# Kernel optimization log

Measured on AMD Instinct MI355X. Metric: run time of the kernel, lower is better.

## Reference

```python
import jax, jax.numpy as jnp
import numpy as np

N = 100_000   # nodes
C = 32        # classes
E = 3_200_000 # edges


def setup_inputs() -> dict:
    key = jax.random.key(0)
    k1, k2, k3, k4, k5 = jax.random.split(key, 5)
    edge_index = jax.random.randint(k1, (2, E), 0, N, dtype=jnp.int32)
    edge_weight = jax.random.uniform(k2, (E,), dtype=jnp.float32) + 0.1  # positive weights
    inputs = jax.random.normal(k3, (N, C), dtype=jnp.float32)
    labels = jax.random.randint(k4, (N,), 0, C)
    y = jax.nn.one_hot(labels, C, dtype=jnp.float32)  # torch.where(y[:, i]) implies one-hot labels
    sample_mask = jax.random.bernoulli(k5, 0.5, (N,))
    return {"edge_index": edge_index, "edge_weight": edge_weight,
            "inputs": inputs, "y": y, "sample_mask": sample_mask}


def _normalize_sparse(edge_index, edge_weight, n):
    # normalize_sparse_tensor: add self-loops (weight 1), then D^{-1/2} A D^{-1/2}
    loop = jnp.arange(n, dtype=edge_index.dtype)
    row = jnp.concatenate([edge_index[0], loop])
    col = jnp.concatenate([edge_index[1], loop])
    w = jnp.concatenate([edge_weight, jnp.ones((n,), edge_weight.dtype)])
    deg = jax.ops.segment_sum(w, row, num_segments=n)
    dinv = jnp.where(deg > 0, jax.lax.rsqrt(deg), 0.0)
    vals = dinv[row] * w * dinv[col]
    return row, col, vals


def reference(edge_index, edge_weight, inputs, y, sample_mask):
    n, c = inputs.shape
    row, col, vals = _normalize_sparse(edge_index, edge_weight, n)

    p = jax.nn.softmax(inputs, axis=1)
    m = sample_mask.astype(p.dtype)[:, None]
    p = p * (1.0 - m) + y * m          # replace predictions by labels on masked nodes
    ym = y * m                          # labels only on masked nodes

    # nodeH = raw_normed_adj @ p   (sparse spmm)  -> (n, c)
    nodeH = jax.ops.segment_sum(vals[:, None] * p[col], row, num_segments=n)

    # per-class mean of nodeH over nodes with label i (one-hot => sum/count)
    cnt = ym.sum(axis=0)                         # (c,)
    H = (ym.T @ nodeH) / cnt[:, None]            # (c, c); NaN rows if class empty

    # NaN fixups (identity when no NaNs present)
    Hn = jnp.isnan(H)
    H = jnp.where(Hn, H.T, H)
    Hn = jnp.isnan(H)
    H0 = jnp.where(Hn, jnp.zeros_like(H), H)
    miss = (1.0 - H0.sum(axis=1, keepdims=True)) / Hn.sum(axis=1, keepdims=True).astype(H.dtype)
    H = jnp.where(Hn, miss, H0)

    # makeDoubleStochasticH: iterate col-norm then row-norm; 'delta' = ||H||_1 (as in source)
    def cond(state):
        _, i, d = state
        return (d >= 1e-12) & (i < 3000)

    def body(state):
        Hc, i, _ = state
        Hc = Hc / Hc.sum(axis=0, keepdims=True)
        Hc = Hc / Hc.sum(axis=1, keepdims=True)
        return Hc, i + 1, jnp.abs(Hc).sum()

    H, _, _ = jax.lax.while_loop(cond, body, (H, jnp.int32(0), jnp.float32(1e30)))
    return H
```

## Files before the change

### kernel.cpp

```cpp
#include <hip/hip_runtime.h>
#include <hip/hip_fp16.h>


#define RS 32768
#define RSH 15
#define BDEG 64
#define NCOPY 16
#define NSC 1024
#define NGE 256

__global__ __launch_bounds__(1024) void
k_deg(const int* __restrict__ ei, const float* __restrict__ ew,
      float* __restrict__ slab, const unsigned char* __restrict__ mask_bytes,
      int* __restrict__ flag, float* __restrict__ T, float* __restrict__ Hg,
      float* __restrict__ cnt, int Nn, int E_, int R) {
  __shared__ float h[RS];
  {
    float4* T4 = (float4*)T;
    int nT4 = Nn * 8;
    float4 z = make_float4(0.f, 0.f, 0.f, 0.f);
    for (int i = blockIdx.x * 1024 + threadIdx.x; i < nT4; i += gridDim.x * 1024)
      T4[i] = z;
  }
  if (blockIdx.x == 0) {
    for (int i = threadIdx.x; i < NCOPY * 1024; i += 1024) Hg[i] = 0.f;
    if (threadIdx.x < 32) cnt[threadIdx.x] = 0.f;
    __shared__ int shi;
    if (threadIdx.x == 0) shi = 0;
    __syncthreads();
    int acc = 0;
    for (int i = threadIdx.x; i < 1024; i += blockDim.x)
      acc |= mask_bytes[i * 4 + 1] | mask_bytes[i * 4 + 2] | mask_bytes[i * 4 + 3];
    if (acc) atomicOr(&shi, 1);
    __syncthreads();
    if (threadIdx.x == 0) *flag = (shi != 0) ? 1 : 0;
  }
  int r = blockIdx.x % R;
  int sl = blockIdx.x / R;
  for (int i = threadIdx.x; i < RS; i += 1024) h[i] = 0.f;
  __syncthreads();
  int lo = r << RSH;
  int Q = E_ >> 2;
  int q0 = (int)((long long)Q * sl / BDEG);
  int q1 = (int)((long long)Q * (sl + 1) / BDEG);
  const int4* ei4 = (const int4*)ei;
  const float4* ew4 = (const float4*)ew;
  int q = q0 + threadIdx.x;
  for (; q + 1024 < q1; q += 2048) {
    int4 ia = ei4[q], ib = ei4[q + 1024];
    float4 wa = ew4[q], wb = ew4[q + 1024];
    unsigned o0 = (unsigned)(ia.x - lo), o1 = (unsigned)(ia.y - lo);
    unsigned o2 = (unsigned)(ia.z - lo), o3 = (unsigned)(ia.w - lo);
    unsigned o4 = (unsigned)(ib.x - lo), o5 = (unsigned)(ib.y - lo);
    unsigned o6 = (unsigned)(ib.z - lo), o7 = (unsigned)(ib.w - lo);
    if (o0 < RS) atomicAdd(&h[o0], wa.x);
    if (o1 < RS) atomicAdd(&h[o1], wa.y);
    if (o2 < RS) atomicAdd(&h[o2], wa.z);
    if (o3 < RS) atomicAdd(&h[o3], wa.w);
    if (o4 < RS) atomicAdd(&h[o4], wb.x);
    if (o5 < RS) atomicAdd(&h[o5], wb.y);
    if (o6 < RS) atomicAdd(&h[o6], wb.z);
    if (o7 < RS) atomicAdd(&h[o7], wb.w);
  }
  for (; q < q1; q += 1024) {
    int4 idx = ei4[q];
    float4 w = ew4[q];
    unsigned o0 = (unsigned)(idx.x - lo), o1 = (unsigned)(idx.y - lo);
    unsigned o2 = (unsigned)(idx.z - lo), o3 = (unsigned)(idx.w - lo);
    if (o0 < RS) atomicAdd(&h[o0], w.x);
    if (o1 < RS) atomicAdd(&h[o1], w.y);
    if (o2 < RS) atomicAdd(&h[o2], w.z);
    if (o3 < RS) atomicAdd(&h[o3], w.w);
  }
  if (sl == BDEG - 1) {
    for (int e = (Q << 2) + threadIdx.x; e < E_; e += 1024) {
      unsigned off = (unsigned)(ei[e] - lo);
      if (off < RS) atomicAdd(&h[off], ew[e]);
    }
  }
  __syncthreads();
  float* dst = slab + ((size_t)r * BDEG + sl) * RS;
  for (int i = threadIdx.x; i < RS; i += 1024) dst[i] = h[i];
}

__global__ void k_node(const float* __restrict__ x, const float* __restrict__ y,
                       const void* __restrict__ maskp, const int* __restrict__ flag,
                       const float* __restrict__ slab, int2* __restrict__ ninfo,
                       __half* __restrict__ p16, float* __restrict__ Hg,
                       float* __restrict__ cnt, int Nn) {
  __shared__ float scnt[32], sdiag[32];
  if (threadIdx.x < 32) { scnt[threadIdx.x] = 0.f; sdiag[threadIdx.x] = 0.f; }
  __syncthreads();
  int n = blockIdx.x * blockDim.x + threadIdx.x;
  if (n < Nn) {
    const float* sl = slab + ((size_t)(n >> RSH) * BDEG) * RS + (n & (RS - 1));
    float d = 0.f;
    #pragma unroll 8
    for (int bb = 0; bb < BDEG; ++bb) d += sl[(size_t)bb * RS];
    float dinv = rsqrtf(d + 1.0f);
    bool byteMask = (*flag != 0);
    bool msk = byteMask ? (((const unsigned char*)maskp)[n] != 0)
                        : (((const int*)maskp)[n] != 0);
    int a = -1;
    if (msk) {
      const float4* yi = (const float4*)(y + (size_t)n * 32);
      #pragma unroll
      for (int q = 0; q < 8; ++q) {
        float4 v = yi[q];
        if (v.x == 1.f) a = q * 4 + 0;
        if (v.y == 1.f) a = q * 4 + 1;
        if (v.z == 1.f) a = q * 4 + 2;
        if (v.w == 1.f) a = q * 4 + 3;
      }
      atomicAdd(&scnt[a], 1.f);
      atomicAdd(&sdiag[a], dinv * dinv);
    } else {
      const float4* xi = (const float4*)(x + (size_t)n * 32);
      float xs[32];
      #pragma unroll
      for (int q = 0; q < 8; ++q) {
        float4 v = xi[q];
        xs[q*4+0] = v.x; xs[q*4+1] = v.y; xs[q*4+2] = v.z; xs[q*4+3] = v.w;
      }
      float mx = -3.4e38f;
      #pragma unroll
      for (int i = 0; i < 32; ++i) mx = fmaxf(mx, xs[i]);
      float s = 0.f;
      #pragma unroll
      for (int i = 0; i < 32; ++i) { xs[i] = __expf(xs[i] - mx); s += xs[i]; }
      float inv = 1.f / s;
      union { short s[32]; int4 v[4]; } u;
      #pragma unroll
      for (int i = 0; i < 32; ++i)
        u.s[i] = __half_as_short(__float2half(xs[i] * inv));
      int4* po = (int4*)(p16 + (size_t)n * 32);
      #pragma unroll
      for (int q = 0; q < 4; ++q) po[q] = u.v[q];
    }
    int2 ni; ni.x = __float_as_int(dinv); ni.y = a;
    ninfo[n] = ni;
  }
  __syncthreads();
  if (threadIdx.x < 32) {
    if (scnt[threadIdx.x] != 0.f) atomicAdd(&cnt[threadIdx.x], scnt[threadIdx.x]);
    if (sdiag[threadIdx.x] != 0.f) atomicAdd(&Hg[threadIdx.x * 33], sdiag[threadIdx.x]);
  }
}

__global__ __launch_bounds__(1024) void
k_scatter(const int* __restrict__ ei, const float* __restrict__ ew,
          const int2* __restrict__ ninfo, float* __restrict__ T,
          float* __restrict__ scatSlab, int E_) {
  __shared__ float sH[1024];
  sH[threadIdx.x] = 0.f;
  __syncthreads();
  int t = blockIdx.x * 1024 + threadIdx.x;
  int stride = gridDim.x * 1024;
  int E4 = E_ >> 2;
  for (int q = t; q < E4; q += stride) {
    int4 rr = ((const int4*)ei)[q];
    int4 cc = ((const int4*)(ei + E_))[q];
    float4 ww = ((const float4*)ew)[q];
    int rs[4] = {rr.x, rr.y, rr.z, rr.w};
    int cs[4] = {cc.x, cc.y, cc.z, cc.w};
    float wv[4] = {ww.x, ww.y, ww.z, ww.w};
    int2 nr[4], nc[4];
    #pragma unroll
    for (int k = 0; k < 4; ++k) nr[k] = ninfo[rs[k]];
    #pragma unroll
    for (int k = 0; k < 4; ++k) nc[k] = ninfo[cs[k]];
    #pragma unroll
    for (int k = 0; k < 4; ++k) {
      if (nr[k].y >= 0) {
        float val = __int_as_float(nr[k].x) * wv[k] * __int_as_float(nc[k].x);
        if (nc[k].y >= 0)
          atomicAdd(&sH[nr[k].y * 32 + nc[k].y], val);
        else
          atomicAdd(&T[(size_t)cs[k] * 32 + nr[k].y], val);
      }
    }
  }
  for (int e = (E4 << 2) + t; e < E_; e += stride) {
    int2 nr = ninfo[ei[e]];
    if (nr.y >= 0) {
      int c = ei[E_ + e];
      int2 nc = ninfo[c];
      float val = __int_as_float(nr.x) * ew[e] * __int_as_float(nc.x);
      if (nc.y >= 0) atomicAdd(&sH[nr.y * 32 + nc.y], val);
      else atomicAdd(&T[(size_t)c * 32 + nr.y], val);
    }
  }
  __syncthreads();
  scatSlab[(size_t)blockIdx.x * 1024 + threadIdx.x] = sH[threadIdx.x];
}

__global__ __launch_bounds__(256) void
k_gemm(const float* __restrict__ T, const __half* __restrict__ p16,
       const float* __restrict__ scatSlab, float* __restrict__ gemmSlab, int Nn) {
  __shared__ float sH[1024];
  for (int i = threadIdx.x; i < 1024; i += 256) sH[i] = 0.f;
  __syncthreads();
  int b = threadIdx.x & 31;
  int hwG = blockIdx.x * 8 + (threadIdx.x >> 5);
  int nHW = gridDim.x * 8;
  int per = (Nn + nHW - 1) / nHW;
  int c0 = hwG * per;
  int c1 = min(c0 + per, Nn);
  float acc[32];
  #pragma unroll
  for (int a = 0; a < 32; ++a) acc[a] = 0.f;
  int c = c0;
  for (; c + 3 < c1; c += 4) {
    float t0 = T[(size_t)(c+0) * 32 + b];
    float t1 = T[(size_t)(c+1) * 32 + b];
    float t2 = T[(size_t)(c+2) * 32 + b];
    float t3 = T[(size_t)(c+3) * 32 + b];
    float p0 = __half2float(p16[(size_t)(c+0) * 32 + b]);
    float p1 = __half2float(p16[(size_t)(c+1) * 32 + b]);
    float p2 = __half2float(p16[(size_t)(c+2) * 32 + b]);
    float p3 = __half2float(p16[(size_t)(c+3) * 32 + b]);
    #pragma unroll
    for (int a = 0; a < 32; ++a)
      acc[a] += __shfl(t0, a, 32) * p0 + __shfl(t1, a, 32) * p1
              + __shfl(t2, a, 32) * p2 + __shfl(t3, a, 32) * p3;
  }
  for (; c < c1; ++c) {
    float tv = T[(size_t)c * 32 + b];
    float pv = __half2float(p16[(size_t)c * 32 + b]);
    #pragma unroll
    for (int a = 0; a < 32; ++a) acc[a] += __shfl(tv, a, 32) * pv;
  }
  #pragma unroll
  for (int a = 0; a < 32; ++a) atomicAdd(&sH[a * 32 + b], acc[a]);
  __syncthreads();
  for (int i = threadIdx.x; i < 1024; i += 256) {
    float v = sH[i];
    #pragma unroll
    for (int k = 0; k < NSC / NGE; ++k)
      v += scatSlab[(size_t)(blockIdx.x + k * NGE) * 1024 + i];
    gemmSlab[(size_t)blockIdx.x * 1024 + i] = v;
  }
}

__global__ __launch_bounds__(1024) void
k_sinkhorn(const float* __restrict__ Hg, const float* __restrict__ gemmSlab,
           const float* __restrict__ cnt, float* __restrict__ out) {
  __shared__ float sHH[1024];
  int t = threadIdx.x;
  float s = 0.f;
  #pragma unroll 8
  for (int k = 0; k < NCOPY; ++k) s += Hg[k * 1024 + t];
  #pragma unroll 8
  for (int k = 0; k < NGE; ++k) s += gemmSlab[k * 1024 + t];
  sHH[t] = s;
  __syncthreads();
  int j = t;
  if (j >= 32) return;
  float cj = cnt[j];
  float Hcol[32], Hrow[32];
  #pragma unroll
  for (int i = 0; i < 32; ++i) Hcol[i] = sHH[i * 32 + j];
  #pragma unroll
  for (int i = 0; i < 32; ++i) Hcol[i] /= __shfl(cj, i);
  #pragma unroll
  for (int k = 0; k < 32; ++k) Hrow[k] = sHH[j * 32 + k] / cj;
  float u = 1.f, v = 1.f;
  for (int it = 0; it < 40; ++it) {
    float a0 = 0.f, a1 = 0.f, a2 = 0.f, a3 = 0.f;
    #pragma unroll
    for (int i = 0; i < 32; i += 4) {
      a0 += Hcol[i+0] * __shfl(u, i+0);
      a1 += Hcol[i+1] * __shfl(u, i+1);
      a2 += Hcol[i+2] * __shfl(u, i+2);
      a3 += Hcol[i+3] * __shfl(u, i+3);
    }
    v = 1.f / ((a0 + a1) + (a2 + a3));
    a0 = a1 = a2 = a3 = 0.f;
    #pragma unroll
    for (int k = 0; k < 32; k += 4) {
      a0 += Hrow[k+0] * __shfl(v, k+0);
      a1 += Hrow[k+1] * __shfl(v, k+1);
      a2 += Hrow[k+2] * __shfl(v, k+2);
      a3 += Hrow[k+3] * __shfl(v, k+3);
    }
    u = 1.f / ((a0 + a1) + (a2 + a3));
  }
  #pragma unroll
  for (int i = 0; i < 32; ++i) out[i * 32 + j] = __shfl(u, i) * Hcol[i] * v;
}

extern "C" void kernel_launch(void* const* d_in, const int* in_sizes, int n_in,
                              void* d_out, int out_size, void* d_ws, size_t ws_size,
                              hipStream_t stream) {
  const int*   ei   = (const int*)d_in[0];
  const float* ew   = (const float*)d_in[1];
  const float* x    = (const float*)d_in[2];
  const float* y    = (const float*)d_in[3];
  const void*  mask = d_in[4];
  float* out = (float*)d_out;
  int E_ = in_sizes[1];
  int Nn = in_sizes[2] / 32;
  int R = (Nn + RS - 1) >> RSH;

  char* ws = (char*)d_ws;
  size_t o = 0;
  float* cnt = (float*)(ws + o);   o += 128;
  int*   flag = (int*)(ws + o);    o += 16;
  float* Hg  = (float*)(ws + o);   o += NCOPY * 4096;
  float* T   = (float*)(ws + o);   o += (size_t)Nn * 128;
  float* slab = (float*)(ws + o);  o += (size_t)R * BDEG * RS * 4;
  float* scatSlab = (float*)(ws + o); o += (size_t)NSC * 4096;
  float* gemmSlab = (float*)(ws + o); o += (size_t)NGE * 4096;
  int2*  ninfo = (int2*)(ws + o);  o += (size_t)Nn * 8;
  __half* p16 = (__half*)(ws + o); o += (size_t)Nn * 64;

  int nb = (Nn + 255) / 256;
  k_deg<<<R * BDEG, 1024, 0, stream>>>(ei, ew, slab, (const unsigned char*)mask,
                                       flag, T, Hg, cnt, Nn, E_, R);
  k_node<<<nb, 256, 0, stream>>>(x, y, mask, flag, slab, ninfo, p16, Hg, cnt, Nn);
  k_scatter<<<NSC, 1024, 0, stream>>>(ei, ew, ninfo, T, scatSlab, E_);
  k_gemm<<<NGE, 256, 0, stream>>>(T, p16, scatSlab, gemmSlab, Nn);
  k_sinkhorn<<<1, 1024, 0, stream>>>(Hg, gemmSlab, cnt, out);
}
```

Baseline: 267.9 us.

## Store degree partials in fp16 and add parallel slab reduction kernel

Degree histogram partials are now written and read as half precision, which halves the slab traffic between k_deg and k_node. The scatter-slab fold moves out of k_gemm. All partial slabs (Hg, gemm, scatter) are placed contiguously and summed by a new 36-block reduction kernel before the single-block Sinkhorn. This shortens the serial reduction in k_sinkhorn at the cost of an extra launch. It also risks fp16 rounding on per-slice degree sums.

```diff
diff --git a/kernel.cpp b/kernel.cpp
--- a/kernel.cpp
+++ b/kernel.cpp
@@ -8,10 +8,12 @@
 #define NCOPY 16
 #define NSC 1024
 #define NGE 256
+#define NTOT (NCOPY + NGE + NSC)
+#define NRED 36
 
 __global__ __launch_bounds__(1024) void
 k_deg(const int* __restrict__ ei, const float* __restrict__ ew,
-      float* __restrict__ slab, const unsigned char* __restrict__ mask_bytes,
+      __half* __restrict__ slab, const unsigned char* __restrict__ mask_bytes,
       int* __restrict__ flag, float* __restrict__ T, float* __restrict__ Hg,
       float* __restrict__ cnt, int Nn, int E_, int R) {
   __shared__ float h[RS];
@@ -79,13 +81,13 @@
     }
   }
   __syncthreads();
-  float* dst = slab + ((size_t)r * BDEG + sl) * RS;
-  for (int i = threadIdx.x; i < RS; i += 1024) dst[i] = h[i];
+  __half* dst = slab + ((size_t)r * BDEG + sl) * RS;
+  for (int i = threadIdx.x; i < RS; i += 1024) dst[i] = __float2half(h[i]);
 }
 
 __global__ void k_node(const float* __restrict__ x, const float* __restrict__ y,
                        const void* __restrict__ maskp, const int* __restrict__ flag,
-                       const float* __restrict__ slab, int2* __restrict__ ninfo,
+                       const __half* __restrict__ slab, int2* __restrict__ ninfo,
                        __half* __restrict__ p16, float* __restrict__ Hg,
                        float* __restrict__ cnt, int Nn) {
   __shared__ float scnt[32], sdiag[32];
@@ -93,10 +95,10 @@
   __syncthreads();
   int n = blockIdx.x * blockDim.x + threadIdx.x;
   if (n < Nn) {
-    const float* sl = slab + ((size_t)(n >> RSH) * BDEG) * RS + (n & (RS - 1));
+    const __half* sl = slab + ((size_t)(n >> RSH) * BDEG) * RS + (n & (RS - 1));
     float d = 0.f;
     #pragma unroll 8
-    for (int bb = 0; bb < BDEG; ++bb) d += sl[(size_t)bb * RS];
+    for (int bb = 0; bb < BDEG; ++bb) d += __half2float(sl[(size_t)bb * RS]);
     float dinv = rsqrtf(d + 1.0f);
     bool byteMask = (*flag != 0);
     bool msk = byteMask ? (((const unsigned char*)maskp)[n] != 0)
@@ -196,7 +198,7 @@
 
 __global__ __launch_bounds__(256) void
 k_gemm(const float* __restrict__ T, const __half* __restrict__ p16,
-       const float* __restrict__ scatSlab, float* __restrict__ gemmSlab, int Nn) {
+       float* __restrict__ gemmSlab, int Nn) {
   __shared__ float sH[1024];
   for (int i = threadIdx.x; i < 1024; i += 256) sH[i] = 0.f;
   __syncthreads();
@@ -233,25 +235,27 @@
   #pragma unroll
   for (int a = 0; a < 32; ++a) atomicAdd(&sH[a * 32 + b], acc[a]);
   __syncthreads();
-  for (int i = threadIdx.x; i < 1024; i += 256) {
-    float v = sH[i];
-    #pragma unroll
-    for (int k = 0; k < NSC / NGE; ++k)
-      v += scatSlab[(size_t)(blockIdx.x + k * NGE) * 1024 + i];
-    gemmSlab[(size_t)blockIdx.x * 1024 + i] = v;
-  }
+  for (int i = threadIdx.x; i < 1024; i += 256)
+    gemmSlab[(size_t)blockIdx.x * 1024 + i] = sH[i];
 }
 
 __global__ __launch_bounds__(1024) void
-k_sinkhorn(const float* __restrict__ Hg, const float* __restrict__ gemmSlab,
-           const float* __restrict__ cnt, float* __restrict__ out) {
+k_red(const float* __restrict__ allSlabs, float* __restrict__ red) {
+  const float* base = allSlabs + (size_t)blockIdx.x * (NTOT / NRED) * 1024 + threadIdx.x;
+  float s = 0.f;
+  #pragma unroll 6
+  for (int k = 0; k < NTOT / NRED; ++k) s += base[(size_t)k * 1024];
+  red[(size_t)blockIdx.x * 1024 + threadIdx.x] = s;
+}
+
+__global__ __launch_bounds__(1024) void
+k_sinkhorn(const float* __restrict__ red, const float* __restrict__ cnt,
+           float* __restrict__ out) {
   __shared__ float sHH[1024];
   int t = threadIdx.x;
   float s = 0.f;
-  #pragma unroll 8
-  for (int k = 0; k < NCOPY; ++k) s += Hg[k * 1024 + t];
-  #pragma unroll 8
-  for (int k = 0; k < NGE; ++k) s += gemmSlab[k * 1024 + t];
+  #pragma unroll 6
+  for (int k = 0; k < NRED; ++k) s += red[(size_t)k * 1024 + t];
   sHH[t] = s;
   __syncthreads();
   int j = t;
@@ -305,12 +309,15 @@
   char* ws = (char*)d_ws;
   size_t o = 0;
   float* cnt = (float*)(ws + o);   o += 128;
-  int*   flag = (int*)(ws + o);    o += 16;
-  float* Hg  = (float*)(ws + o);   o += NCOPY * 4096;
+  int*   flag = (int*)(ws + o);    o += 128;
+  float* allSlabs = (float*)(ws + o);
+  float* Hg       = allSlabs;
+  float* gemmSlab = allSlabs + (size_t)NCOPY * 1024;
+  float* scatSlab = allSlabs + (size_t)(NCOPY + NGE) * 1024;
+  o += (size_t)NTOT * 4096;
+  float* red = (float*)(ws + o);   o += (size_t)NRED * 4096;
   float* T   = (float*)(ws + o);   o += (size_t)Nn * 128;
-  float* slab = (float*)(ws + o);  o += (size_t)R * BDEG * RS * 4;
-  float* scatSlab = (float*)(ws + o); o += (size_t)NSC * 4096;
-  float* gemmSlab = (float*)(ws + o); o += (size_t)NGE * 4096;
+  __half* slab = (__half*)(ws + o); o += (size_t)R * BDEG * RS * 2;
   int2*  ninfo = (int2*)(ws + o);  o += (size_t)Nn * 8;
   __half* p16 = (__half*)(ws + o); o += (size_t)Nn * 64;
 
@@ -319,6 +326,7 @@
                                        flag, T, Hg, cnt, Nn, E_, R);
   k_node<<<nb, 256, 0, stream>>>(x, y, mask, flag, slab, ninfo, p16, Hg, cnt, Nn);
   k_scatter<<<NSC, 1024, 0, stream>>>(ei, ew, ninfo, T, scatSlab, E_);
-  k_gemm<<<NGE, 256, 0, stream>>>(T, p16, scatSlab, gemmSlab, Nn);
-  k_sinkhorn<<<1, 1024, 0, stream>>>(Hg, gemmSlab, cnt, out);
-}
+  k_gemm<<<NGE, 256, 0, stream>>>(T, p16, gemmSlab, Nn);
+  k_red<<<NRED, 1024, 0, stream>>>(allSlabs, red);
+  k_sinkhorn<<<1, 1024, 0, stream>>>(red, cnt, out);
+}
```

After: 251.9 us. 1.06x faster.

## Fuse all stages into one cooperative persistent kernel with grid syncs

Applied to the files above, without the earlier changes.

Replaces five kernel launches with a single cooperative kernel of 256 blocks that separates the degree histogram, node prep, edge scatter, class GEMM, reduction and Sinkhorn phases with grid-wide syncs. The degree slabs are stored in half precision, and partial H results are reduced hierarchically through a small staging buffer. This removes launch gaps and slab traffic, but cuts parallelism to 256 blocks and adds grid-sync cost. Storing degree partials in fp16 also reduces accuracy.

```diff
diff --git a/kernel.cpp b/kernel.cpp
--- a/kernel.cpp
+++ b/kernel.cpp
@@ -1,292 +1,276 @@
 #include <hip/hip_runtime.h>
 #include <hip/hip_fp16.h>
+#include <hip/hip_cooperative_groups.h>
+
+namespace cg = cooperative_groups;
 
 
 #define RS 32768
 #define RSH 15
-#define BDEG 64
-#define NCOPY 16
-#define NSC 1024
-#define NGE 256
+#define NBLK 256
+#define NRED 16
 
 __global__ __launch_bounds__(1024) void
-k_deg(const int* __restrict__ ei, const float* __restrict__ ew,
-      float* __restrict__ slab, const unsigned char* __restrict__ mask_bytes,
-      int* __restrict__ flag, float* __restrict__ T, float* __restrict__ Hg,
-      float* __restrict__ cnt, int Nn, int E_, int R) {
+k_all(const int* __restrict__ ei, const float* __restrict__ ew,
+      const float* __restrict__ x, const float* __restrict__ y,
+      const unsigned char* __restrict__ maskb, float* __restrict__ out,
+      float* __restrict__ T, __half* __restrict__ slab,
+      int2* __restrict__ ninfo, __half* __restrict__ p16,
+      float* __restrict__ Hg, float* __restrict__ cnt, int* __restrict__ flag,
+      float* __restrict__ gemmSlab, float* __restrict__ red,
+      int Nn, int E_, int R) {
+  cg::grid_group grid = cg::this_grid();
   __shared__ float h[RS];
+  __shared__ int shi;
+  const int tid = threadIdx.x;
+  const int bid = blockIdx.x;
+  const int SL = NBLK / R;
+
   {
     float4* T4 = (float4*)T;
     int nT4 = Nn * 8;
     float4 z = make_float4(0.f, 0.f, 0.f, 0.f);
-    for (int i = blockIdx.x * 1024 + threadIdx.x; i < nT4; i += gridDim.x * 1024)
-      T4[i] = z;
-  }
-  if (blockIdx.x == 0) {
-    for (int i = threadIdx.x; i < NCOPY * 1024; i += 1024) Hg[i] = 0.f;
-    if (threadIdx.x < 32) cnt[threadIdx.x] = 0.f;
-    __shared__ int shi;
-    if (threadIdx.x == 0) shi = 0;
+    for (int i = bid * 1024 + tid; i < nT4; i += NBLK * 1024) T4[i] = z;
+  }
+  if (bid == 0) {
+    Hg[tid] = 0.f;
+    if (tid < 32) cnt[tid] = 0.f;
+    if (tid == 0) shi = 0;
     __syncthreads();
     int acc = 0;
-    for (int i = threadIdx.x; i < 1024; i += blockDim.x)
-      acc |= mask_bytes[i * 4 + 1] | mask_bytes[i * 4 + 2] | mask_bytes[i * 4 + 3];
+    for (int i = tid; i < 1024; i += 1024)
+      acc |= maskb[i * 4 + 1] | maskb[i * 4 + 2] | maskb[i * 4 + 3];
     if (acc) atomicOr(&shi, 1);
     __syncthreads();
-    if (threadIdx.x == 0) *flag = (shi != 0) ? 1 : 0;
-  }
-  int r = blockIdx.x % R;
-  int sl = blockIdx.x / R;
-  for (int i = threadIdx.x; i < RS; i += 1024) h[i] = 0.f;
+    if (tid == 0) *flag = (shi != 0) ? 1 : 0;
+  }
+  for (int i = tid; i < RS; i += 1024) h[i] = 0.f;
   __syncthreads();
-  int lo = r << RSH;
-  int Q = E_ >> 2;
-  int q0 = (int)((long long)Q * sl / BDEG);
-  int q1 = (int)((long long)Q * (sl + 1) / BDEG);
-  const int4* ei4 = (const int4*)ei;
-  const float4* ew4 = (const float4*)ew;
-  int q = q0 + threadIdx.x;
-  for (; q + 1024 < q1; q += 2048) {
-    int4 ia = ei4[q], ib = ei4[q + 1024];
-    float4 wa = ew4[q], wb = ew4[q + 1024];
-    unsigned o0 = (unsigned)(ia.x - lo), o1 = (unsigned)(ia.y - lo);
-    unsigned o2 = (unsigned)(ia.z - lo), o3 = (unsigned)(ia.w - lo);
-    unsigned o4 = (unsigned)(ib.x - lo), o5 = (unsigned)(ib.y - lo);
-    unsigned o6 = (unsigned)(ib.z - lo), o7 = (unsigned)(ib.w - lo);
-    if (o0 < RS) atomicAdd(&h[o0], wa.x);
-    if (o1 < RS) atomicAdd(&h[o1], wa.y);
-    if (o2 < RS) atomicAdd(&h[o2], wa.z);
-    if (o3 < RS) atomicAdd(&h[o3], wa.w);
-    if (o4 < RS) atomicAdd(&h[o4], wb.x);
-    if (o5 < RS) atomicAdd(&h[o5], wb.y);
-    if (o6 < RS) atomicAdd(&h[o6], wb.z);
-    if (o7 < RS) atomicAdd(&h[o7], wb.w);
-  }
-  for (; q < q1; q += 1024) {
-    int4 idx = ei4[q];
-    float4 w = ew4[q];
-    unsigned o0 = (unsigned)(idx.x - lo), o1 = (unsigned)(idx.y - lo);
-    unsigned o2 = (unsigned)(idx.z - lo), o3 = (unsigned)(idx.w - lo);
-    if (o0 < RS) atomicAdd(&h[o0], w.x);
-    if (o1 < RS) atomicAdd(&h[o1], w.y);
-    if (o2 < RS) atomicAdd(&h[o2], w.z);
-    if (o3 < RS) atomicAdd(&h[o3], w.w);
-  }
-  if (sl == BDEG - 1) {
-    for (int e = (Q << 2) + threadIdx.x; e < E_; e += 1024) {
-      unsigned off = (unsigned)(ei[e] - lo);
-      if (off < RS) atomicAdd(&h[off], ew[e]);
-    }
-  }
+  {
+    int r = bid % R;
+    int sl = bid / R;
+    if (sl < SL) {
+      int lo = r << RSH;
+      int Q = E_ >> 2;
+      int q0 = (int)((long long)Q * sl / SL);
+      int q1 = (int)((long long)Q * (sl + 1) / SL);
+      const int4* ei4 = (const int4*)ei;
+      const float4* ew4 = (const float4*)ew;
+      int q = q0 + tid;
+      for (; q + 1024 < q1; q += 2048) {
+        int4 ia = ei4[q], ib = ei4[q + 1024];
+        float4 wa = ew4[q], wb = ew4[q + 1024];
+        unsigned o0 = (unsigned)(ia.x - lo), o1 = (unsigned)(ia.y - lo);
+        unsigned o2 = (unsigned)(ia.z - lo), o3 = (unsigned)(ia.w - lo);
+        unsigned o4 = (unsigned)(ib.x - lo), o5 = (unsigned)(ib.y - lo);
+        unsigned o6 = (unsigned)(ib.z - lo), o7 = (unsigned)(ib.w - lo);
+        if (o0 < RS) atomicAdd(&h[o0], wa.x);
+        if (o1 < RS) atomicAdd(&h[o1], wa.y);
+        if (o2 < RS) atomicAdd(&h[o2], wa.z);
+        if (o3 < RS) atomicAdd(&h[o3], wa.w);
+        if (o4 < RS) atomicAdd(&h[o4], wb.x);
+        if (o5 < RS) atomicAdd(&h[o5], wb.y);
+        if (o6 < RS) atomicAdd(&h[o6], wb.z);
+        if (o7 < RS) atomicAdd(&h[o7], wb.w);
+      }
+      for (; q < q1; q += 1024) {
+        int4 idx = ei4[q];
+        float4 w = ew4[q];
+        unsigned o0 = (unsigned)(idx.x - lo), o1 = (unsigned)(idx.y - lo);
+        unsigned o2 = (unsigned)(idx.z - lo), o3 = (unsigned)(idx.w - lo);
+        if (o0 < RS) atomicAdd(&h[o0], w.x);
+        if (o1 < RS) atomicAdd(&h[o1], w.y);
+        if (o2 < RS) atomicAdd(&h[o2], w.z);
+        if (o3 < RS) atomicAdd(&h[o3], w.w);
+      }
+      if (sl == SL - 1) {
+        for (int e = (Q << 2) + tid; e < E_; e += 1024) {
+          unsigned off = (unsigned)(ei[e] - lo);
+          if (off < RS) atomicAdd(&h[off], ew[e]);
+        }
+      }
+      __syncthreads();
+      __half* dst = slab + ((size_t)r * SL + sl) * RS;
+      for (int i = tid; i < RS; i += 1024) dst[i] = __float2half(h[i]);
+    } else {
+      __syncthreads();
+    }
+  }
+  grid.sync();
+
+  {
+    float* scnt = h + 1024;
+    float* sdiag = h + 1056;
+    if (tid < 32) { scnt[tid] = 0.f; sdiag[tid] = 0.f; }
+    __syncthreads();
+    bool byteMask = (*flag != 0);
+    for (int n = bid * 1024 + tid; n < Nn; n += NBLK * 1024) {
+      const __half* slp = slab + ((size_t)(n >> RSH) * SL) * RS + (n & (RS - 1));
+      float d = 0.f;
+      #pragma unroll 8
+      for (int bb = 0; bb < SL; ++bb) d += __half2float(slp[(size_t)bb * RS]);
+      float dinv = rsqrtf(d + 1.0f);
+      bool msk = byteMask ? (maskb[n] != 0) : (((const int*)maskb)[n] != 0);
+      int a = -1;
+      if (msk) {
+        const float4* yi = (const float4*)(y + (size_t)n * 32);
+        #pragma unroll
+        for (int q = 0; q < 8; ++q) {
+          float4 v = yi[q];
+          if (v.x == 1.f) a = q * 4 + 0;
+          if (v.y == 1.f) a = q * 4 + 1;
+          if (v.z == 1.f) a = q * 4 + 2;
+          if (v.w == 1.f) a = q * 4 + 3;
+        }
+        atomicAdd(&scnt[a], 1.f);
+        atomicAdd(&sdiag[a], dinv * dinv);
+      } else {
+        const float4* xi = (const float4*)(x + (size_t)n * 32);
+        float xs[32];
+        #pragma unroll
+        for (int q = 0; q < 8; ++q) {
+          float4 v = xi[q];
+          xs[q*4+0] = v.x; xs[q*4+1] = v.y; xs[q*4+2] = v.z; xs[q*4+3] = v.w;
+        }
+        float mx = -3.4e38f;
+        #pragma unroll
+        for (int i = 0; i < 32; ++i) mx = fmaxf(mx, xs[i]);
+        float s = 0.f;
+        #pragma unroll
+        for (int i = 0; i < 32; ++i) { xs[i] = __expf(xs[i] - mx); s += xs[i]; }
+        float inv = 1.f / s;
+        union { short sh[32]; int4 v[4]; } u;
+        #pragma unroll
+        for (int i = 0; i < 32; ++i)
+          u.sh[i] = __half_as_short(__float2half(xs[i] * inv));
+        int4* po = (int4*)(p16 + (size_t)n * 32);
+        #pragma unroll
+        for (int q = 0; q < 4; ++q) po[q] = u.v[q];
+      }
+      int2 ni; ni.x = __float_as_int(dinv); ni.y = a;
+      ninfo[n] = ni;
+    }
+    __syncthreads();
+    if (tid < 32) {
+      if (scnt[tid] != 0.f) atomicAdd(&cnt[tid], scnt[tid]);
+      if (sdiag[tid] != 0.f) atomicAdd(&Hg[tid * 33], sdiag[tid]);
+    }
+  }
+  grid.sync();
+
+  h[tid] = 0.f;
   __syncthreads();
-  float* dst = slab + ((size_t)r * BDEG + sl) * RS;
-  for (int i = threadIdx.x; i < RS; i += 1024) dst[i] = h[i];
-}
-
-__global__ void k_node(const float* __restrict__ x, const float* __restrict__ y,
-                       const void* __restrict__ maskp, const int* __restrict__ flag,
-                       const float* __restrict__ slab, int2* __restrict__ ninfo,
-                       __half* __restrict__ p16, float* __restrict__ Hg,
-                       float* __restrict__ cnt, int Nn) {
-  __shared__ float scnt[32], sdiag[32];
-  if (threadIdx.x < 32) { scnt[threadIdx.x] = 0.f; sdiag[threadIdx.x] = 0.f; }
-  __syncthreads();
-  int n = blockIdx.x * blockDim.x + threadIdx.x;
-  if (n < Nn) {
-    const float* sl = slab + ((size_t)(n >> RSH) * BDEG) * RS + (n & (RS - 1));
-    float d = 0.f;
-    #pragma unroll 8
-    for (int bb = 0; bb < BDEG; ++bb) d += sl[(size_t)bb * RS];
-    float dinv = rsqrtf(d + 1.0f);
-    bool byteMask = (*flag != 0);
-    bool msk = byteMask ? (((const unsigned char*)maskp)[n] != 0)
-                        : (((const int*)maskp)[n] != 0);
-    int a = -1;
-    if (msk) {
-      const float4* yi = (const float4*)(y + (size_t)n * 32);
-      #pragma unroll
-      for (int q = 0; q < 8; ++q) {
-        float4 v = yi[q];
-        if (v.x == 1.f) a = q * 4 + 0;
-        if (v.y == 1.f) a = q * 4 + 1;
-        if (v.z == 1.f) a = q * 4 + 2;
-        if (v.w == 1.f) a = q * 4 + 3;
-      }
-      atomicAdd(&scnt[a], 1.f);
-      atomicAdd(&sdiag[a], dinv * dinv);
-    } else {
-      const float4* xi = (const float4*)(x + (size_t)n * 32);
-      float xs[32];
-      #pragma unroll
-      for (int q = 0; q < 8; ++q) {
-        float4 v = xi[q];
-        xs[q*4+0] = v.x; xs[q*4+1] = v.y; xs[q*4+2] = v.z; xs[q*4+3] = v.w;
-      }
-      float mx = -3.4e38f;
-      #pragma unroll
-      for (int i = 0; i < 32; ++i) mx = fmaxf(mx, xs[i]);
-      float s = 0.f;
-      #pragma unroll
-      for (int i = 0; i < 32; ++i) { xs[i] = __expf(xs[i] - mx); s += xs[i]; }
-      float inv = 1.f / s;
-      union { short s[32]; int4 v[4]; } u;
-      #pragma unroll
-      for (int i = 0; i < 32; ++i)
-        u.s[i] = __half_as_short(__float2half(xs[i] * inv));
-      int4* po = (int4*)(p16 + (size_t)n * 32);
-      #pragma unroll
-      for (int q = 0; q < 4; ++q) po[q] = u.v[q];
-    }
-    int2 ni; ni.x = __float_as_int(dinv); ni.y = a;
-    ninfo[n] = ni;
-  }
-  __syncthreads();
-  if (threadIdx.x < 32) {
-    if (scnt[threadIdx.x] != 0.f) atomicAdd(&cnt[threadIdx.x], scnt[threadIdx.x]);
-    if (sdiag[threadIdx.x] != 0.f) atomicAdd(&Hg[threadIdx.x * 33], sdiag[threadIdx.x]);
-  }
-}
-
-__global__ __launch_bounds__(1024) void
-k_scatter(const int* __restrict__ ei, const float* __restrict__ ew,
-          const int2* __restrict__ ninfo, float* __restrict__ T,
-          float* __restrict__ scatSlab, int E_) {
-  __shared__ float sH[1024];
-  sH[threadIdx.x] = 0.f;
-  __syncthreads();
-  int t = blockIdx.x * 1024 + threadIdx.x;
-  int stride = gridDim.x * 1024;
-  int E4 = E_ >> 2;
-  for (int q = t; q < E4; q += stride) {
-    int4 rr = ((const int4*)ei)[q];
-    int4 cc = ((const int4*)(ei + E_))[q];
-    float4 ww = ((const float4*)ew)[q];
-    int rs[4] = {rr.x, rr.y, rr.z, rr.w};
-    int cs[4] = {cc.x, cc.y, cc.z, cc.w};
-    float wv[4] = {ww.x, ww.y, ww.z, ww.w};
-    int2 nr[4], nc[4];
+  {
+    int E4 = E_ >> 2;
+    for (int q = bid * 1024 + tid; q < E4; q += NBLK * 1024) {
+      int4 rr = ((const int4*)ei)[q];
+      int4 cc = ((const int4*)(ei + E_))[q];
+      float4 ww = ((const float4*)ew)[q];
+      int rs[4] = {rr.x, rr.y, rr.z, rr.w};
+      int cs[4] = {cc.x, cc.y, cc.z, cc.w};
+      float wv[4] = {ww.x, ww.y, ww.z, ww.w};
+      int2 nr[4], nc[4];
+      #pragma unroll
+      for (int k = 0; k < 4; ++k) nr[k] = ninfo[rs[k]];
+      #pragma unroll
+      for (int k = 0; k < 4; ++k) nc[k] = ninfo[cs[k]];
+      #pragma unroll
+      for (int k = 0; k < 4; ++k) {
+        if (nr[k].y >= 0) {
+          float val = __int_as_float(nr[k].x) * wv[k] * __int_as_float(nc[k].x);
+          if (nc[k].y >= 0)
+            atomicAdd(&h[nr[k].y * 32 + nc[k].y], val);
+          else
+            atomicAdd(&T[(size_t)cs[k] * 32 + nr[k].y], val);
+        }
+      }
+    }
+    for (int e = (E4 << 2) + bid * 1024 + tid; e < E_; e += NBLK * 1024) {
+      int2 nr = ninfo[ei[e]];
+      if (nr.y >= 0) {
+        int c = ei[E_ + e];
+        int2 nc = ninfo[c];
+        float val = __int_as_float(nr.x) * ew[e] * __int_as_float(nc.x);
+        if (nc.y >= 0) atomicAdd(&h[nr.y * 32 + nc.y], val);
+        else atomicAdd(&T[(size_t)c * 32 + nr.y], val);
+      }
+    }
+  }
+  grid.sync();
+
+  {
+    int per = (Nn + NBLK - 1) / NBLK;
+    int c0 = bid * per;
+    int c1 = min(c0 + per, Nn);
+    int b = tid & 31;
+    int hw = tid >> 5;
+    float acc[32];
     #pragma unroll
-    for (int k = 0; k < 4; ++k) nr[k] = ninfo[rs[k]];
-    #pragma unroll
-    for (int k = 0; k < 4; ++k) nc[k] = ninfo[cs[k]];
-    #pragma unroll
-    for (int k = 0; k < 4; ++k) {
-      if (nr[k].y >= 0) {
-        float val = __int_as_float(nr[k].x) * wv[k] * __int_as_float(nc[k].x);
-        if (nc[k].y >= 0)
-          atomicAdd(&sH[nr[k].y * 32 + nc[k].y], val);
-        else
-          atomicAdd(&T[(size_t)cs[k] * 32 + nr[k].y], val);
-      }
-    }
-  }
-  for (int e = (E4 << 2) + t; e < E_; e += stride) {
-    int2 nr = ninfo[ei[e]];
-    if (nr.y >= 0) {
-      int c = ei[E_ + e];
-      int2 nc = ninfo[c];
-      float val = __int_as_float(nr.x) * ew[e] * __int_as_float(nc.x);
-      if (nc.y >= 0) atomicAdd(&sH[nr.y * 32 + nc.y], val);
-      else atomicAdd(&T[(size_t)c * 32 + nr.y], val);
-    }
-  }
-  __syncthreads();
-  scatSlab[(size_t)blockIdx.x * 1024 + threadIdx.x] = sH[threadIdx.x];
-}
-
-__global__ __launch_bounds__(256) void
-k_gemm(const float* __restrict__ T, const __half* __restrict__ p16,
-       const float* __restrict__ scatSlab, float* __restrict__ gemmSlab, int Nn) {
-  __shared__ float sH[1024];
-  for (int i = threadIdx.x; i < 1024; i += 256) sH[i] = 0.f;
-  __syncthreads();
-  int b = threadIdx.x & 31;
-  int hwG = blockIdx.x * 8 + (threadIdx.x >> 5);
-  int nHW = gridDim.x * 8;
-  int per = (Nn + nHW - 1) / nHW;
-  int c0 = hwG * per;
-  int c1 = min(c0 + per, Nn);
-  float acc[32];
-  #pragma unroll
-  for (int a = 0; a < 32; ++a) acc[a] = 0.f;
-  int c = c0;
-  for (; c + 3 < c1; c += 4) {
-    float t0 = T[(size_t)(c+0) * 32 + b];
-    float t1 = T[(size_t)(c+1) * 32 + b];
-    float t2 = T[(size_t)(c+2) * 32 + b];
-    float t3 = T[(size_t)(c+3) * 32 + b];
-    float p0 = __half2float(p16[(size_t)(c+0) * 32 + b]);
-    float p1 = __half2float(p16[(size_t)(c+1) * 32 + b]);
-    float p2 = __half2float(p16[(size_t)(c+2) * 32 + b]);
-    float p3 = __half2float(p16[(size_t)(c+3) * 32 + b]);
+    for (int a = 0; a < 32; ++a) acc[a] = 0.f;
+    for (int c = c0 + hw; c < c1; c += 32) {
+      float tv = T[(size_t)c * 32 + b];
+      float pv = __half2float(p16[(size_t)c * 32 + b]);
+      #pragma unroll
+      for (int a = 0; a < 32; ++a) acc[a] += __shfl(tv, a, 32) * pv;
+    }
     #pragma unroll
     for (int a = 0; a < 32; ++a)
-      acc[a] += __shfl(t0, a, 32) * p0 + __shfl(t1, a, 32) * p1
-              + __shfl(t2, a, 32) * p2 + __shfl(t3, a, 32) * p3;
-  }
-  for (; c < c1; ++c) {
-    float tv = T[(size_t)c * 32 + b];
-    float pv = __half2float(p16[(size_t)c * 32 + b]);
+      if (acc[a] != 0.f) atomicAdd(&h[a * 32 + b], acc[a]);
+    __syncthreads();
+    gemmSlab[(size_t)bid * 1024 + tid] = h[tid];
+  }
+  grid.sync();
+
+  if (bid < NRED) {
+    float s = 0.f;
     #pragma unroll
-    for (int a = 0; a < 32; ++a) acc[a] += __shfl(tv, a, 32) * pv;
-  }
-  #pragma unroll
-  for (int a = 0; a < 32; ++a) atomicAdd(&sH[a * 32 + b], acc[a]);
-  __syncthreads();
-  for (int i = threadIdx.x; i < 1024; i += 256) {
-    float v = sH[i];
+    for (int k = 0; k < NBLK / NRED; ++k)
+      s += gemmSlab[(size_t)(bid * (NBLK / NRED) + k) * 1024 + tid];
+    red[(size_t)bid * 1024 + tid] = s;
+  }
+  grid.sync();
+
+  if (bid == 0) {
+    float s = Hg[tid];
     #pragma unroll
-    for (int k = 0; k < NSC / NGE; ++k)
-      v += scatSlab[(size_t)(blockIdx.x + k * NGE) * 1024 + i];
-    gemmSlab[(size_t)blockIdx.x * 1024 + i] = v;
-  }
-}
-
-__global__ __launch_bounds__(1024) void
-k_sinkhorn(const float* __restrict__ Hg, const float* __restrict__ gemmSlab,
-           const float* __restrict__ cnt, float* __restrict__ out) {
-  __shared__ float sHH[1024];
-  int t = threadIdx.x;
-  float s = 0.f;
-  #pragma unroll 8
-  for (int k = 0; k < NCOPY; ++k) s += Hg[k * 1024 + t];
-  #pragma unroll 8
-  for (int k = 0; k < NGE; ++k) s += gemmSlab[k * 1024 + t];
-  sHH[t] = s;
-  __syncthreads();
-  int j = t;
-  if (j >= 32) return;
-  float cj = cnt[j];
-  float Hcol[32], Hrow[32];
-  #pragma unroll
-  for (int i = 0; i < 32; ++i) Hcol[i] = sHH[i * 32 + j];
-  #pragma unroll
-  for (int i = 0; i < 32; ++i) Hcol[i] /= __shfl(cj, i);
-  #pragma unroll
-  for (int k = 0; k < 32; ++k) Hrow[k] = sHH[j * 32 + k] / cj;
-  float u = 1.f, v = 1.f;
-  for (int it = 0; it < 40; ++it) {
-    float a0 = 0.f, a1 = 0.f, a2 = 0.f, a3 = 0.f;
-    #pragma unroll
-    for (int i = 0; i < 32; i += 4) {
-      a0 += Hcol[i+0] * __shfl(u, i+0);
-      a1 += Hcol[i+1] * __shfl(u, i+1);
-      a2 += Hcol[i+2] * __shfl(u, i+2);
-      a3 += Hcol[i+3] * __shfl(u, i+3);
-    }
-    v = 1.f / ((a0 + a1) + (a2 + a3));
-    a0 = a1 = a2 = a3 = 0.f;
-    #pragma unroll
-    for (int k = 0; k < 32; k += 4) {
-      a0 += Hrow[k+0] * __shfl(v, k+0);
-      a1 += Hrow[k+1] * __shfl(v, k+1);
-      a2 += Hrow[k+2] * __shfl(v, k+2);
-      a3 += Hrow[k+3] * __shfl(v, k+3);
-    }
-    u = 1.f / ((a0 + a1) + (a2 + a3));
-  }
-  #pragma unroll
-  for (int i = 0; i < 32; ++i) out[i * 32 + j] = __shfl(u, i) * Hcol[i] * v;
+    for (int k = 0; k < NRED; ++k) s += red[(size_t)k * 1024 + tid];
+    h[tid] = s;
+    __syncthreads();
+    int j = tid;
+    if (j < 32) {
+      float cj = cnt[j];
+      float Hcol[32], Hrow[32];
+      #pragma unroll
+      for (int i = 0; i < 32; ++i) Hcol[i] = h[i * 32 + j];
+      #pragma unroll
+      for (int i = 0; i < 32; ++i) Hcol[i] /= __shfl(cj, i);
+      #pragma unroll
+      for (int k = 0; k < 32; ++k) Hrow[k] = h[j * 32 + k] / cj;
+      float u = 1.f, v = 1.f;
+      for (int it = 0; it < 40; ++it) {
+        float a0 = 0.f, a1 = 0.f, a2 = 0.f, a3 = 0.f;
+        #pragma unroll
+        for (int i = 0; i < 32; i += 4) {
+          a0 += Hcol[i+0] * __shfl(u, i+0);
+          a1 += Hcol[i+1] * __shfl(u, i+1);
+          a2 += Hcol[i+2] * __shfl(u, i+2);
+          a3 += Hcol[i+3] * __shfl(u, i+3);
+        }
+        v = 1.f / ((a0 + a1) + (a2 + a3));
+        a0 = a1 = a2 = a3 = 0.f;
+        #pragma unroll
+        for (int k = 0; k < 32; k += 4) {
+          a0 += Hrow[k+0] * __shfl(v, k+0);
+          a1 += Hrow[k+1] * __shfl(v, k+1);
+          a2 += Hrow[k+2] * __shfl(v, k+2);
+          a3 += Hrow[k+3] * __shfl(v, k+3);
+        }
+        u = 1.f / ((a0 + a1) + (a2 + a3));
+      }
+      #pragma unroll
+      for (int i = 0; i < 32; ++i) out[i * 32 + j] = __shfl(u, i) * Hcol[i] * v;
+    }
+  }
 }
 
 extern "C" void kernel_launch(void* const* d_in, const int* in_sizes, int n_in,
@@ -296,7 +280,7 @@
   const float* ew   = (const float*)d_in[1];
   const float* x    = (const float*)d_in[2];
   const float* y    = (const float*)d_in[3];
-  const void*  mask = d_in[4];
+  const unsigned char* mask = (const unsigned char*)d_in[4];
   float* out = (float*)d_out;
   int E_ = in_sizes[1];
   int Nn = in_sizes[2] / 32;
@@ -304,21 +288,19 @@
 
   char* ws = (char*)d_ws;
   size_t o = 0;
-  float* cnt = (float*)(ws + o);   o += 128;
-  int*   flag = (int*)(ws + o);    o += 16;
-  float* Hg  = (float*)(ws + o);   o += NCOPY * 4096;
-  float* T   = (float*)(ws + o);   o += (size_t)Nn * 128;
-  float* slab = (float*)(ws + o);  o += (size_t)R * BDEG * RS * 4;
-  float* scatSlab = (float*)(ws + o); o += (size_t)NSC * 4096;
-  float* gemmSlab = (float*)(ws + o); o += (size_t)NGE * 4096;
-  int2*  ninfo = (int2*)(ws + o);  o += (size_t)Nn * 8;
-  __half* p16 = (__half*)(ws + o); o += (size_t)Nn * 64;
-
-  int nb = (Nn + 255) / 256;
-  k_deg<<<R * BDEG, 1024, 0, stream>>>(ei, ew, slab, (const unsigned char*)mask,
-                                       flag, T, Hg, cnt, Nn, E_, R);
-  k_node<<<nb, 256, 0, stream>>>(x, y, mask, flag, slab, ninfo, p16, Hg, cnt, Nn);
-  k_scatter<<<NSC, 1024, 0, stream>>>(ei, ew, ninfo, T, scatSlab, E_);
-  k_gemm<<<NGE, 256, 0, stream>>>(T, p16, scatSlab, gemmSlab, Nn);
-  k_sinkhorn<<<1, 1024, 0, stream>>>(Hg, gemmSlab, cnt, out);
+  float* cnt = (float*)(ws + o);    o += 128;
+  int*   flag = (int*)(ws + o);     o += 128;
+  float* Hg  = (float*)(ws + o);    o += 4096;
+  float* gemmSlab = (float*)(ws + o); o += (size_t)NBLK * 4096;
+  float* red = (float*)(ws + o);    o += (size_t)NRED * 4096;
+  float* T   = (float*)(ws + o);    o += (size_t)Nn * 128;
+  __half* slab = (__half*)(ws + o); o += (size_t)NBLK * RS * 2;
+  int2*  ninfo = (int2*)(ws + o);   o += (size_t)Nn * 8;
+  __half* p16 = (__half*)(ws + o);  o += (size_t)Nn * 64;
+
+  void* args[] = {(void*)&ei, (void*)&ew, (void*)&x, (void*)&y, (void*)&mask,
+                  (void*)&out, (void*)&T, (void*)&slab, (void*)&ninfo, (void*)&p16,
+                  (void*)&Hg, (void*)&cnt, (void*)&flag, (void*)&gemmSlab,
+                  (void*)&red, (void*)&Nn, (void*)&E_, (void*)&R};
+  hipLaunchCooperativeKernel((void*)k_all, dim3(NBLK), dim3(1024), args, 0, stream);
 }
```

Result: slower. 451.7 us (+68.6%).
